# Performance work log

Hardware: AMD Instinct MI355X
Metric: run time of the kernel (lower is better)

The kernel has to match this reference:

```python
import jax, jax.numpy as jnp
import numpy as np

WS = 8          # window size -> N = 64
SHIFT = 4       # shift size for shifted windows
FEAT = 32       # feature map H = W at stage 3
C = 512         # channels (SwinV2-B stage 3)
HEADS = 16
B_IMG = 128     # images -> 128 * (32/8)^2 = 2048 windows


def _rel_coords_table():
    # log-spaced continuous relative coords table, SwinV2 style: [(2W-1)^2, 2]
    r = np.arange(-(WS - 1), WS, dtype=np.float32)
    t = np.stack(np.meshgrid(r, r, indexing='ij'), axis=-1)  # [15,15,2]
    t = t / (WS - 1) * 8.0
    t = np.sign(t) * np.log2(np.abs(t) + 1.0) / np.log2(8.0)
    return t.reshape(-1, 2)


def _rel_pos_index():
    c = np.stack(np.meshgrid(np.arange(WS), np.arange(WS), indexing='ij'))  # [2,8,8]
    cf = c.reshape(2, -1)
    rel = (cf[:, :, None] - cf[:, None, :]).transpose(1, 2, 0)  # [64,64,2]
    rel[:, :, 0] += WS - 1
    rel[:, :, 1] += WS - 1
    rel[:, :, 0] *= 2 * WS - 1
    return rel.sum(-1).astype(np.int32)  # [64,64]


def _shift_mask():
    # standard SwinV2 shifted-window attention mask: [nW, N, N] in {0, -100}
    img = np.zeros((FEAT, FEAT), dtype=np.float32)
    cnt = 0
    for hs in (slice(0, -WS), slice(-WS, -SHIFT), slice(-SHIFT, None)):
        for ws in (slice(0, -WS), slice(-WS, -SHIFT), slice(-SHIFT, None)):
            img[hs, ws] = cnt
            cnt += 1
    win = img.reshape(FEAT // WS, WS, FEAT // WS, WS).transpose(0, 2, 1, 3)
    win = win.reshape(-1, WS * WS)  # [nW, 64]
    diff = win[:, None, :] - win[:, :, None]
    return np.where(diff != 0, -100.0, 0.0).astype(np.float32)


def setup_inputs() -> dict:
    key = jax.random.key(0)
    ks = jax.random.split(key, 10)
    nW = (FEAT // WS) ** 2  # 16 windows per image
    Bw = B_IMG * nW         # 2048
    N = WS * WS
    s = 0.02
    return {
        'x': jax.random.normal(ks[0], (Bw, N, C), jnp.float32),
        'mask': jnp.asarray(_shift_mask()),
        'qkv_w': jax.random.normal(ks[1], (3 * C, C), jnp.float32) * s,
        'q_bias': jnp.zeros((C,), jnp.float32),
        'v_bias': jnp.zeros((C,), jnp.float32),
        'logit_scale': jnp.full((HEADS, 1, 1), np.log(10.0), jnp.float32),
        'cpb_w1': jax.random.normal(ks[2], (512, 2), jnp.float32) * s,
        'cpb_b1': jnp.zeros((512,), jnp.float32),
        'cpb_w2': jax.random.normal(ks[3], (HEADS, 512), jnp.float32) * s,
        'proj_w': jax.random.normal(ks[4], (C, C), jnp.float32) * s,
        'proj_b': jnp.zeros((C,), jnp.float32),
        'rel_coords_table': jnp.asarray(_rel_coords_table()),
        'rel_pos_index': jnp.asarray(_rel_pos_index()),
    }


def reference(x, mask, qkv_w, q_bias, v_bias, logit_scale, cpb_w1, cpb_b1,
              cpb_w2, proj_w, proj_b, rel_coords_table, rel_pos_index):
    Bw, N, Cdim = x.shape
    H = logit_scale.shape[0]
    d = Cdim // H
    # qkv projection; k has no bias (SwinV2)
    qkv_bias = jnp.concatenate([q_bias, jnp.zeros_like(q_bias), v_bias])
    qkv = (x @ qkv_w.T + qkv_bias).reshape(Bw, N, 3, H, d).transpose(2, 0, 3, 1, 4)
    q, k, v = qkv[0], qkv[1], qkv[2]  # each [Bw,H,N,d]
    # cosine attention with learned per-head temperature
    qn = q / jnp.maximum(jnp.linalg.norm(q, axis=-1, keepdims=True), 1e-12)
    kn = k / jnp.maximum(jnp.linalg.norm(k, axis=-1, keepdims=True), 1e-12)
    attn = jnp.einsum('bhnd,bhmd->bhnm', qn, kn)
    scale = jnp.exp(jnp.minimum(logit_scale, jnp.log(100.0)))  # [H,1,1]
    attn = attn * scale[None]
    # continuous relative position bias via small MLP over log-spaced coords
    tbl = jax.nn.relu(rel_coords_table @ cpb_w1.T + cpb_b1) @ cpb_w2.T  # [(2W-1)^2,H]
    bias = tbl[rel_pos_index.reshape(-1)].reshape(N, N, H).transpose(2, 0, 1)
    attn = attn + 16.0 * jax.nn.sigmoid(bias)[None]
    # shifted-window mask applied per window group
    nW = mask.shape[0]
    attn = attn.reshape(Bw // nW, nW, H, N, N) + mask[None, :, None]
    attn = jax.nn.softmax(attn.reshape(Bw, H, N, N), axis=-1)
    out = jnp.einsum('bhnm,bhmd->bhnd', attn, v)
    out = out.transpose(0, 2, 1, 3).reshape(Bw, N, Cdim)
    return out @ proj_w.T + proj_b
```

## Files before the change

kernel.cpp:

```cpp
#include <hip/hip_runtime.h>
#include <stdint.h>
#include <stddef.h>


typedef __attribute__((ext_vector_type(8))) short bf16x8;
typedef __attribute__((ext_vector_type(4))) float f32x4;
typedef __attribute__((ext_vector_type(4))) unsigned short us4;
typedef __attribute__((ext_vector_type(8))) unsigned short us8;
typedef unsigned short u16;
typedef unsigned int u32;

#define FENCE() asm volatile("" ::: "memory")
#define WAITV4() asm volatile("s_waitcnt vmcnt(4)" ::: "memory")
#define WAITV3() asm volatile("s_waitcnt vmcnt(3)" ::: "memory")
#define WAITV0() asm volatile("s_waitcnt vmcnt(0)" ::: "memory")
#define WAITL0() asm volatile("s_waitcnt lgkmcnt(0)" ::: "memory")

__device__ __forceinline__ u16 f2bf(float f) {
  union { __bf16 b; u16 u; } cv;
  cv.b = (__bf16)f;
  return cv.u;
}
__device__ __forceinline__ float bf2f(u16 s) {
  return __uint_as_float(((u32)s) << 16);
}
__device__ __forceinline__ void gl_lds16(const void* g, void* l) {
  __builtin_amdgcn_global_load_lds(
      (const __attribute__((address_space(1))) u32*)g,
      (__attribute__((address_space(3))) u32*)l, 16, 0, 0);
}
__device__ __forceinline__ f32x4 mfma16(bf16x8 a, bf16x8 b, f32x4 c) {
  return __builtin_amdgcn_mfma_f32_16x16x32_bf16(a, b, c, 0, 0, 0);
}
__device__ __forceinline__ bf16x8 ldswz(const u16* p, int ks) {
  return *(const bf16x8*)((const u16*)((uintptr_t)p ^ (uintptr_t)(ks << 6)));
}


__global__ void conv_w_kernel(const float* __restrict__ QW, const float* __restrict__ PW,
                              u16* __restrict__ WQB, u16* __restrict__ WPB) {
  int idx = blockIdx.x * 256 + threadIdx.x;
  const int NQ = 1536 * 512 / 4;
  float4 v; u16* dst;
  if (idx < NQ) { v = ((const float4*)QW)[idx]; dst = WQB + (size_t)idx * 4; }
  else { int k = idx - NQ; v = ((const float4*)PW)[k]; dst = WPB + (size_t)k * 4; }
  us4 u; u.x = f2bf(v.x); u.y = f2bf(v.y); u.z = f2bf(v.z); u.w = f2bf(v.w);
  *(us4*)dst = u;
}

__global__ void xconv_kernel(const float* __restrict__ X, u16* __restrict__ XB) {
  size_t idx = (size_t)blockIdx.x * 256 + threadIdx.x;
  float4 a = ((const float4*)X)[idx * 2];
  float4 b = ((const float4*)X)[idx * 2 + 1];
  us8 o;
  o[0] = f2bf(a.x); o[1] = f2bf(a.y); o[2] = f2bf(a.z); o[3] = f2bf(a.w);
  o[4] = f2bf(b.x); o[5] = f2bf(b.y); o[6] = f2bf(b.z); o[7] = f2bf(b.w);
  *(us8*)&XB[idx * 8] = o;
}

__global__ void sig16_kernel(const float* __restrict__ CT, const float* __restrict__ W1,
                             const float* __restrict__ B1, const float* __restrict__ W2,
                             float* __restrict__ SIG) {
  int i = blockIdx.x;
  int tid = threadIdx.x;
  float c0 = CT[i * 2 + 0], c1 = CT[i * 2 + 1];
  float a[16];
  #pragma unroll
  for (int hh = 0; hh < 16; ++hh) a[hh] = 0.f;
  #pragma unroll
  for (int jj = 0; jj < 2; ++jj) {
    int j = tid + jj * 256;
    float h = fmaxf(c0 * W1[j * 2 + 0] + c1 * W1[j * 2 + 1] + B1[j], 0.f);
    #pragma unroll
    for (int hh = 0; hh < 16; ++hh) a[hh] += h * W2[hh * 512 + j];
  }
  __shared__ float red[4][16];
  #pragma unroll
  for (int hh = 0; hh < 16; ++hh) {
    float v = a[hh];
    for (int m = 1; m < 64; m <<= 1) v += __shfl_xor(v, m);
    if ((tid & 63) == 0) red[tid >> 6][hh] = v;
  }
  __syncthreads();
  if (tid < 16) {
    float v = red[0][tid] + red[1][tid] + red[2][tid] + red[3][tid];
    SIG[i * 16 + tid] = 16.f / (1.f + __expf(-v));
  }
}

__global__ void cmb_kernel(const float* __restrict__ SIG, const float* __restrict__ MASK,
                           const int* __restrict__ RPI, float* __restrict__ CMB) {
  int b = blockIdx.x;
  int w = b >> 4, h = b & 15;
  int tid = threadIdx.x;
  const float* mrow = &MASK[(size_t)w * 4096];
  float* crow = &CMB[(size_t)b * 4096];
  #pragma unroll
  for (int it = 0; it < 16; ++it) {
    int nm = it * 256 + tid;
    crow[nm] = SIG[RPI[nm] * 16 + h] + mrow[nm];
  }
}


#define GEMM32_KLOOP()                                                     \
  _Pragma("unroll")                                                        \
  for (int t = 0; t < 16; ++t) {                                           \
    const int Sb = (t % 3) * 12288;                                        \
    _Pragma("unroll")                                                      \
    for (int m = 0; m < 4; ++m)                                            \
      af[m] = *(const bf16x8*)&S[Sb + (wm * 64 + m * 16 + fr) * 32 + fsw]; \
    _Pragma("unroll")                                                      \
    for (int n = 0; n < 2; ++n)                                            \
      bf[n] = *(const bf16x8*)&S[Sb + 4096 + (wn * 64 + n * 16 + fr) * 32 + fsw]; \
    if (t + 2 <= 15) stageB(t + 2);                                        \
    FENCE(); __builtin_amdgcn_s_barrier(); FENCE();                        \
    WAITL0(); __builtin_amdgcn_sched_barrier(0);                           \
    __builtin_amdgcn_s_setprio(1);                                         \
    _Pragma("unroll")                                                      \
    for (int m = 0; m < 4; ++m)                                            \
      _Pragma("unroll")                                                    \
      for (int n = 0; n < 2; ++n)                                          \
        acc[m][n] = mfma16(af[m], bf[n], acc[m][n]);                       \
    __builtin_amdgcn_s_setprio(0);                                         \
    FENCE(); __builtin_amdgcn_s_barrier(); FENCE();                        \
    _Pragma("unroll")                                                      \
    for (int n = 0; n < 2; ++n)                                            \
      bf[n] = *(const bf16x8*)&S[Sb + 4096 + (wn * 64 + (n + 2) * 16 + fr) * 32 + fsw]; \
    if (t + 3 <= 15) stageA(t + 3);                                        \
    if (t <= 12) { WAITV4(); }                                             \
    else if (t == 13) { WAITV3(); }                                        \
    else if (t == 14) { WAITV0(); }                                        \
    FENCE(); __builtin_amdgcn_s_barrier(); FENCE();                        \
    WAITL0(); __builtin_amdgcn_sched_barrier(0);                           \
    __builtin_amdgcn_s_setprio(1);                                         \
    _Pragma("unroll")                                                      \
    for (int m = 0; m < 4; ++m)                                            \
      _Pragma("unroll")                                                    \
      for (int n = 0; n < 2; ++n)                                          \
        acc[m][n + 2] = mfma16(af[m], bf[n], acc[m][n + 2]);               \
    __builtin_amdgcn_s_setprio(0);                                         \
    FENCE(); __builtin_amdgcn_s_barrier(); FENCE();                        \
  }


__global__ __launch_bounds__(512, 4) void qkv_g32(
    const u16* __restrict__ XB, const u16* __restrict__ WB,
    const float* __restrict__ QB, const float* __restrict__ VB,
    u16* __restrict__ QKV) {
  __shared__ u16 S[36864];
  const int tid = threadIdx.x, lane = tid & 63, w = tid >> 6;
  int bid = blockIdx.x;
  int swz = (bid & 7) * 768 + (bid >> 3);
  const int mt = swz / 6, nt = swz - mt * 6;
  const long m0 = (long)mt * 128, n0 = (long)nt * 256;
  const int wm = w >> 2, wn = w & 3;
  const int fr = lane & 15, lg = lane >> 4;
  const int fsw = (lg ^ ((fr >> 1) & 3)) << 3;
  const f32x4 zf = {0.f, 0.f, 0.f, 0.f};

  f32x4 acc[4][4];
  #pragma unroll
  for (int mi = 0; mi < 4; ++mi)
    #pragma unroll
    for (int ni = 0; ni < 4; ++ni) acc[mi][ni] = zf;

  const int arow = tid >> 2;
  const int asc = (tid & 3) ^ ((arow >> 1) & 3);
  const u16* aSrc = &XB[(size_t)(m0 + arow) * 512 + asc * 8];
  const u16* bSrc0 = &WB[(size_t)(n0 + arow) * 512 + asc * 8];
  const u16* bSrc1 = &WB[(size_t)(n0 + 128 + arow) * 512 + asc * 8];

  auto stageA = [&](int kt) {
    gl_lds16(aSrc + kt * 32, &S[(kt % 3) * 12288 + w * 512]);
  };
  auto stageB = [&](int kt) {
    gl_lds16(bSrc0 + kt * 32, &S[(kt % 3) * 12288 + 4096 + w * 512]);
    gl_lds16(bSrc1 + kt * 32, &S[(kt % 3) * 12288 + 8192 + w * 512]);
  };

  bf16x8 af[4], bf[2];

  stageA(0); stageB(0); stageA(1); stageB(1); stageA(2);
  WAITV4();
  FENCE(); __builtin_amdgcn_s_barrier(); FENCE();

  GEMM32_KLOOP()

  u16* eb = &S[w * 4608];
  #pragma unroll
  for (int ni = 0; ni < 4; ++ni) {
    const long c = n0 + wn * 64 + ni * 16 + fr;
    float bias = (c < 512) ? QB[c] : (c < 1024 ? 0.f : VB[c - 1024]);
    #pragma unroll
    for (int mi = 0; mi < 4; ++mi)
      #pragma unroll
      for (int r = 0; r < 4; ++r)
        eb[(mi * 16 + lg * 4 + r) * 72 + ni * 16 + fr] = f2bf(acc[mi][ni][r] + bias);
  }
  WAITL0();
  #pragma unroll
  for (int i = 0; i < 8; ++i) {
    int row = i * 8 + (lane >> 3);
    int c16 = lane & 7;
    us8 v = *(const us8*)&eb[row * 72 + c16 * 8];
    *(us8*)&QKV[(size_t)(m0 + wm * 64 + row) * 1536 + n0 + wn * 64 + c16 * 8] = v;
  }
}


__global__ __launch_bounds__(512, 4) void proj_g32(
    const u16* __restrict__ A, const u16* __restrict__ WB,
    const float* __restrict__ PB, float* __restrict__ OUT) {
  __shared__ u16 S[36864];
  const int tid = threadIdx.x, lane = tid & 63, w = tid >> 6;
  int bid = blockIdx.x;
  int swz = (bid & 7) * 256 + (bid >> 3);
  const int mt = swz >> 1, nt = swz & 1;
  const long m0 = (long)mt * 128, n0 = (long)nt * 256;
  const int wm = w >> 2, wn = w & 3;
  const int fr = lane & 15, lg = lane >> 4;
  const int fsw = (lg ^ ((fr >> 1) & 3)) << 3;
  const f32x4 zf = {0.f, 0.f, 0.f, 0.f};

  f32x4 acc[4][4];
  #pragma unroll
  for (int mi = 0; mi < 4; ++mi)
    #pragma unroll
    for (int ni = 0; ni < 4; ++ni) acc[mi][ni] = zf;

  const int arow = tid >> 2;
  const int asc = (tid & 3) ^ ((arow >> 1) & 3);
  const u16* aSrc = &A[(size_t)(m0 + arow) * 1536 + asc * 8];
  const u16* bSrc0 = &WB[(size_t)(n0 + arow) * 512 + asc * 8];
  const u16* bSrc1 = &WB[(size_t)(n0 + 128 + arow) * 512 + asc * 8];

  auto stageA = [&](int kt) {
    gl_lds16(aSrc + kt * 32, &S[(kt % 3) * 12288 + w * 512]);
  };
  auto stageB = [&](int kt) {
    gl_lds16(bSrc0 + kt * 32, &S[(kt % 3) * 12288 + 4096 + w * 512]);
    gl_lds16(bSrc1 + kt * 32, &S[(kt % 3) * 12288 + 8192 + w * 512]);
  };

  bf16x8 af[4], bf[2];

  stageA(0); stageB(0); stageA(1); stageB(1); stageA(2);
  WAITV4();
  FENCE(); __builtin_amdgcn_s_barrier(); FENCE();

  GEMM32_KLOOP()

  #pragma unroll
  for (int ni = 0; ni < 4; ++ni) {
    const long c = n0 + wn * 64 + ni * 16 + fr;
    float bias = PB[c];
    #pragma unroll
    for (int mi = 0; mi < 4; ++mi)
      #pragma unroll
      for (int r = 0; r < 4; ++r) {
        long row = m0 + wm * 64 + mi * 16 + lg * 4 + r;
        OUT[row * 512 + c] = acc[mi][ni][r] + bias;
      }
  }
}


__global__ __launch_bounds__(256, 2) void qkv_gemm_rs(
    const float* __restrict__ X, const u16* __restrict__ WB,
    const float* __restrict__ QB, const float* __restrict__ VB,
    u16* __restrict__ QKV) {
  __shared__ u16 As[128 * 64];
  __shared__ u16 Bs[128 * 64];
  const int tid = threadIdx.x, lane = tid & 63, w = tid >> 6;
  int bid = blockIdx.x;
  int swz = (bid & 7) * 1536 + (bid >> 3);
  const int mt = swz / 12, nt = swz - mt * 12;
  const long m0 = (long)mt * 128, n0 = (long)nt * 128;
  const int wm = w >> 1, wn = w & 1;
  const f32x4 zf = {0.f, 0.f, 0.f, 0.f};

  f32x4 acc[4][4];
  #pragma unroll
  for (int mi = 0; mi < 4; ++mi)
    #pragma unroll
    for (int ni = 0; ni < 4; ++ni) acc[mi][ni] = zf;

  const int fr = lane & 15;
  const int fsw = ((lane >> 4) ^ (lane & 7)) * 8;
  const u16* Ap = &As[(wm * 64 + fr) * 64 + fsw];
  const u16* Bp = &Bs[(wn * 64 + fr) * 64 + fsw];

  for (int t = 0; t < 8; ++t) {
    float4 av[8];
    #pragma unroll
    for (int i = 0; i < 8; ++i) {
      int ch = tid + (i << 8);
      int row = ch >> 4, kc = ch & 15;
      av[i] = *(const float4*)&X[(m0 + row) * 512 + t * 64 + kc * 4];
    }
    #pragma unroll
    for (int i = 0; i < 4; ++i) {
      int ch = ((w << 2) + i) * 64 + lane;
      int row = ch >> 3, kc = (ch & 7) ^ (row & 7);
      gl_lds16(&WB[(n0 + row) * 512 + t * 64 + kc * 8], &Bs[((w << 2) + i) * 512]);
    }
    #pragma unroll
    for (int i = 0; i < 8; ++i) {
      int ch = tid + (i << 8);
      int row = ch >> 4, kc = ch & 15;
      int kcs = kc ^ ((row & 7) << 1);
      us4 u; u.x = f2bf(av[i].x); u.y = f2bf(av[i].y); u.z = f2bf(av[i].z); u.w = f2bf(av[i].w);
      *(us4*)&As[row * 64 + kcs * 4] = u;
    }
    __syncthreads();
    #pragma unroll
    for (int ks = 0; ks < 2; ++ks) {
      bf16x8 af[4], bfr[4];
      #pragma unroll
      for (int mi = 0; mi < 4; ++mi) af[mi] = ldswz(Ap + mi * 1024, ks);
      #pragma unroll
      for (int ni = 0; ni < 4; ++ni) bfr[ni] = ldswz(Bp + ni * 1024, ks);
      #pragma unroll
      for (int mi = 0; mi < 4; ++mi)
        #pragma unroll
        for (int ni = 0; ni < 4; ++ni)
          acc[mi][ni] = mfma16(af[mi], bfr[ni], acc[mi][ni]);
    }
    __syncthreads();
  }

  #pragma unroll
  for (int ni = 0; ni < 4; ++ni) {
    const long c = n0 + wn * 64 + ni * 16 + (lane & 15);
    float bias = (c < 512) ? QB[c] : (c < 1024 ? 0.f : VB[c - 1024]);
    #pragma unroll
    for (int mi = 0; mi < 4; ++mi)
      #pragma unroll
      for (int r = 0; r < 4; ++r) {
        long row = m0 + wm * 64 + mi * 16 + (lane >> 4) * 4 + r;
        QKV[row * 1536 + c] = f2bf(acc[mi][ni][r] + bias);
      }
  }
}


__global__ __launch_bounds__(256, 4) void attn_kernel(
    u16* __restrict__ QKV, const float* __restrict__ CMB, const float* __restrict__ LS) {
  __shared__ u16 sm[7424];
  u16* qs = sm;
  u16* ksm = sm + 2560;
  u16* ps = sm;
  u16* vt = sm + 5120;
  const int tid = threadIdx.x, lane = tid & 63, w = tid >> 6;
  const int b = blockIdx.x, wi = b & 15;
  const size_t base = (size_t)b * 64 * 1536;
  const int cl = lane & 15, lg = lane >> 4;
  const int srow = tid >> 2, sck = tid & 3;
  const int vd = tid & 31, vkb = tid >> 5;
  const f32x4 zf = {0.f, 0.f, 0.f, 0.f};

  for (int h = 0; h < 16; ++h) {
    const float scale = __expf(fminf(LS[h], 4.6051702f));
    {
      us8 qv = *(const us8*)&QKV[base + (size_t)srow * 1536 + h * 32 + sck * 8];
      float qf[8]; float ss = 0.f;
      #pragma unroll
      for (int j = 0; j < 8; ++j) { qf[j] = bf2f(qv[j]); ss += qf[j] * qf[j]; }
      ss += __shfl_xor(ss, 1); ss += __shfl_xor(ss, 2);
      float rn = scale / fmaxf(sqrtf(ss), 1e-12f);
      us8 qo;
      #pragma unroll
      for (int j = 0; j < 8; ++j) qo[j] = f2bf(qf[j] * rn);
      *(us8*)&qs[srow * 40 + sck * 8] = qo;
    }
    {
      us8 kv = *(const us8*)&QKV[base + (size_t)srow * 1536 + 512 + h * 32 + sck * 8];
      float kf[8]; float ss = 0.f;
      #pragma unroll
      for (int j = 0; j < 8; ++j) { kf[j] = bf2f(kv[j]); ss += kf[j] * kf[j]; }
      ss += __shfl_xor(ss, 1); ss += __shfl_xor(ss, 2);
      float rn = 1.f / fmaxf(sqrtf(ss), 1e-12f);
      us8 ko;
      #pragma unroll
      for (int j = 0; j < 8; ++j) ko[j] = f2bf(kf[j] * rn);
      *(us8*)&ksm[srow * 40 + sck * 8] = ko;
    }
    {
      us8 vo;
      #pragma unroll
      for (int e = 0; e < 8; ++e)
        vo[e] = QKV[base + (size_t)(vkb * 8 + e) * 1536 + 1024 + h * 32 + vd];
      *(us8*)&vt[vd * 72 + vkb * 8] = vo;
    }
    __syncthreads();

    bf16x8 aq = *(const bf16x8*)&qs[(w * 16 + cl) * 40 + lg * 8];
    f32x4 s4[4];
    #pragma unroll
    for (int nt = 0; nt < 4; ++nt) {
      bf16x8 bk = *(const bf16x8*)&ksm[(nt * 16 + cl) * 40 + lg * 8];
      s4[nt] = mfma16(aq, bk, zf);
    }

    const float* cp = &CMB[((size_t)(wi * 16 + h)) << 12];
    const int r0 = w * 16 + lg * 4;
    float p[4][4];
    #pragma unroll
    for (int r = 0; r < 4; ++r) {
      float mx = -3.0e38f;
      #pragma unroll
      for (int q4 = 0; q4 < 4; ++q4) {
        float v = s4[q4][r] + cp[(r0 + r) * 64 + q4 * 16 + cl];
        p[q4][r] = v; mx = fmaxf(mx, v);
      }
      mx = fmaxf(mx, __shfl_xor(mx, 1));
      mx = fmaxf(mx, __shfl_xor(mx, 2));
      mx = fmaxf(mx, __shfl_xor(mx, 4));
      mx = fmaxf(mx, __shfl_xor(mx, 8));
      float sum = 0.f;
      #pragma unroll
      for (int q4 = 0; q4 < 4; ++q4) { float e = __expf(p[q4][r] - mx); p[q4][r] = e; sum += e; }
      sum += __shfl_xor(sum, 1); sum += __shfl_xor(sum, 2);
      sum += __shfl_xor(sum, 4); sum += __shfl_xor(sum, 8);
      float inv = 1.f / sum;
      #pragma unroll
      for (int q4 = 0; q4 < 4; ++q4) p[q4][r] *= inv;
    }
    __syncthreads();

    #pragma unroll
    for (int r = 0; r < 4; ++r)
      #pragma unroll
      for (int q4 = 0; q4 < 4; ++q4)
        ps[(r0 + r) * 72 + q4 * 16 + cl] = f2bf(p[q4][r]);

    f32x4 o4[2]; o4[0] = zf; o4[1] = zf;
    #pragma unroll
    for (int ks = 0; ks < 2; ++ks) {
      bf16x8 ap = *(const bf16x8*)&ps[(w * 16 + cl) * 72 + ks * 32 + lg * 8];
      #pragma unroll
      for (int n2 = 0; n2 < 2; ++n2) {
        bf16x8 bv = *(const bf16x8*)&vt[(n2 * 16 + cl) * 72 + ks * 32 + lg * 8];
        o4[n2] = mfma16(ap, bv, o4[n2]);
      }
    }
    #pragma unroll
    for (int n2 = 0; n2 < 2; ++n2)
      #pragma unroll
      for (int r = 0; r < 4; ++r)
        QKV[base + (size_t)(w * 16 + lg * 4 + r) * 1536 + h * 32 + n2 * 16 + cl] = f2bf(o4[n2][r]);
    __syncthreads();
  }
}


extern "C" void kernel_launch(void* const* d_in, const int* in_sizes, int n_in,
                              void* d_out, int out_size, void* d_ws, size_t ws_size,
                              hipStream_t stream) {
  const float* X    = (const float*)d_in[0];
  const float* MASK = (const float*)d_in[1];
  const float* QW   = (const float*)d_in[2];
  const float* QB   = (const float*)d_in[3];
  const float* VB   = (const float*)d_in[4];
  const float* LS   = (const float*)d_in[5];
  const float* CW1  = (const float*)d_in[6];
  const float* CB1  = (const float*)d_in[7];
  const float* CW2  = (const float*)d_in[8];
  const float* PW   = (const float*)d_in[9];
  const float* PB   = (const float*)d_in[10];
  const float* CT   = (const float*)d_in[11];
  const int*   RPI  = (const int*)d_in[12];
  float* OUT = (float*)d_out;

  char* ws = (char*)d_ws;
  const bool big = ws_size >= 543178752ull;
  u16* QKV = (u16*)ws;
  u16* XB  = (u16*)(ws + 402653184ull);
  size_t off = big ? 536870912ull : 402653184ull;
  float* CMB = (float*)(ws + off);  off += 4194304ull;
  float* SIG = (float*)(ws + off);  off += 16384ull;
  u16*   WQB = (u16*)(ws + off);    off += 1572864ull;
  u16*   WPB = (u16*)(ws + off);

  conv_w_kernel<<<1024, 256, 0, stream>>>(QW, PW, WQB, WPB);
  sig16_kernel<<<225, 256, 0, stream>>>(CT, CW1, CB1, CW2, SIG);
  cmb_kernel<<<256, 256, 0, stream>>>(SIG, MASK, RPI, CMB);
  if (big) {
    xconv_kernel<<<32768, 256, 0, stream>>>(X, XB);
    qkv_g32<<<6144, 512, 0, stream>>>(XB, WQB, QB, VB, QKV);
  } else {
    qkv_gemm_rs<<<12288, 256, 0, stream>>>(X, WQB, QB, VB, QKV);
  }
  attn_kernel<<<2048, 256, 0, stream>>>(QKV, CMB, LS);
  proj_g32<<<2048, 512, 0, stream>>>(QKV, WPB, PB, OUT);
}
```

Measured before the change: 641.9 us.

## Assign one head per wavefront in attention, removing block-wide syncs

The attention kernel is restructured so each wavefront owns a whole (window, head) pair: 4 heads per block, 8192 blocks, instead of one block looping over 16 heads with 4 waves splitting rows. Q/K are loaded and normalized directly into MFMA register fragments, the bias/mask is preloaded into the accumulators, and only P and V^T go through per-wave LDS, so all __syncthreads are dropped. This aims to remove the serial head loop and barrier stalls, and to expose more parallelism and overlap of memory latency. In exchange, register pressure and LDS use go up (launch bounds lowered to 3 blocks per CU), and V is transposed through scalar LDS writes.

```diff
diff --git a/kernel.cpp b/kernel.cpp
--- a/kernel.cpp
+++ b/kernel.cpp
@@ -345,113 +345,124 @@
 }
 
 
-__global__ __launch_bounds__(256, 4) void attn_kernel(
+__global__ __launch_bounds__(256, 3) void attn_wh(
     u16* __restrict__ QKV, const float* __restrict__ CMB, const float* __restrict__ LS) {
-  __shared__ u16 sm[7424];
-  u16* qs = sm;
-  u16* ksm = sm + 2560;
-  u16* ps = sm;
-  u16* vt = sm + 5120;
+  __shared__ u16 smu[26112];
   const int tid = threadIdx.x, lane = tid & 63, w = tid >> 6;
-  const int b = blockIdx.x, wi = b & 15;
-  const size_t base = (size_t)b * 64 * 1536;
-  const int cl = lane & 15, lg = lane >> 4;
-  const int srow = tid >> 2, sck = tid & 3;
-  const int vd = tid & 31, vkb = tid >> 5;
+  const int b = blockIdx.x;
+  const int win = b >> 2;
+  const int h = (b & 3) * 4 + w;
+  const int wi = win & 15;
+  const size_t base = (size_t)win * 64 * 1536;
+  const int fr = lane & 15, lg = lane >> 4;
+  u16* ps = &smu[w * 6528];
+  u16* vt = ps + 4352;
+  const float scale = __expf(fminf(LS[h], 4.6051702f));
+  const float* cp = &CMB[((size_t)(wi * 16 + h)) << 12];
   const f32x4 zf = {0.f, 0.f, 0.f, 0.f};
 
-  for (int h = 0; h < 16; ++h) {
-    const float scale = __expf(fminf(LS[h], 4.6051702f));
-    {
-      us8 qv = *(const us8*)&QKV[base + (size_t)srow * 1536 + h * 32 + sck * 8];
-      float qf[8]; float ss = 0.f;
-      #pragma unroll
-      for (int j = 0; j < 8; ++j) { qf[j] = bf2f(qv[j]); ss += qf[j] * qf[j]; }
-      ss += __shfl_xor(ss, 1); ss += __shfl_xor(ss, 2);
-      float rn = scale / fmaxf(sqrtf(ss), 1e-12f);
-      us8 qo;
-      #pragma unroll
-      for (int j = 0; j < 8; ++j) qo[j] = f2bf(qf[j] * rn);
-      *(us8*)&qs[srow * 40 + sck * 8] = qo;
-    }
-    {
-      us8 kv = *(const us8*)&QKV[base + (size_t)srow * 1536 + 512 + h * 32 + sck * 8];
-      float kf[8]; float ss = 0.f;
-      #pragma unroll
-      for (int j = 0; j < 8; ++j) { kf[j] = bf2f(kv[j]); ss += kf[j] * kf[j]; }
-      ss += __shfl_xor(ss, 1); ss += __shfl_xor(ss, 2);
-      float rn = 1.f / fmaxf(sqrtf(ss), 1e-12f);
-      us8 ko;
-      #pragma unroll
-      for (int j = 0; j < 8; ++j) ko[j] = f2bf(kf[j] * rn);
-      *(us8*)&ksm[srow * 40 + sck * 8] = ko;
-    }
-    {
-      us8 vo;
-      #pragma unroll
-      for (int e = 0; e < 8; ++e)
-        vo[e] = QKV[base + (size_t)(vkb * 8 + e) * 1536 + 1024 + h * 32 + vd];
-      *(us8*)&vt[vd * 72 + vkb * 8] = vo;
-    }
-    __syncthreads();
-
-    bf16x8 aq = *(const bf16x8*)&qs[(w * 16 + cl) * 40 + lg * 8];
-    f32x4 s4[4];
-    #pragma unroll
-    for (int nt = 0; nt < 4; ++nt) {
-      bf16x8 bk = *(const bf16x8*)&ksm[(nt * 16 + cl) * 40 + lg * 8];
-      s4[nt] = mfma16(aq, bk, zf);
-    }
-
-    const float* cp = &CMB[((size_t)(wi * 16 + h)) << 12];
-    const int r0 = w * 16 + lg * 4;
-    float p[4][4];
+  us8 vrow[4];
+  #pragma unroll
+  for (int c = 0; c < 4; ++c)
+    vrow[c] = *(const us8*)&QKV[base + (size_t)lane * 1536 + 1024 + h * 32 + c * 8];
+
+  f32x4 acc[4][4];
+  #pragma unroll
+  for (int m = 0; m < 4; ++m)
+    #pragma unroll
+    for (int n = 0; n < 4; ++n)
+      #pragma unroll
+      for (int r = 0; r < 4; ++r)
+        acc[m][n][r] = cp[(m * 16 + lg * 4 + r) * 64 + n * 16 + fr];
+
+  bf16x8 af[4], bk[4];
+  #pragma unroll
+  for (int m = 0; m < 4; ++m) {
+    us8 qv = *(const us8*)&QKV[base + (size_t)(m * 16 + fr) * 1536 + h * 32 + lg * 8];
+    float qf[8]; float ss = 0.f;
+    #pragma unroll
+    for (int j = 0; j < 8; ++j) { qf[j] = bf2f(qv[j]); ss += qf[j] * qf[j]; }
+    ss += __shfl_xor(ss, 16); ss += __shfl_xor(ss, 32);
+    float rn = scale / fmaxf(sqrtf(ss), 1e-12f);
+    union { us8 u; bf16x8 b; } cv;
+    #pragma unroll
+    for (int j = 0; j < 8; ++j) cv.u[j] = f2bf(qf[j] * rn);
+    af[m] = cv.b;
+  }
+  #pragma unroll
+  for (int m = 0; m < 4; ++m) {
+    us8 kv = *(const us8*)&QKV[base + (size_t)(m * 16 + fr) * 1536 + 512 + h * 32 + lg * 8];
+    float kf[8]; float ss = 0.f;
+    #pragma unroll
+    for (int j = 0; j < 8; ++j) { kf[j] = bf2f(kv[j]); ss += kf[j] * kf[j]; }
+    ss += __shfl_xor(ss, 16); ss += __shfl_xor(ss, 32);
+    float rn = 1.f / fmaxf(sqrtf(ss), 1e-12f);
+    union { us8 u; bf16x8 b; } cv;
+    #pragma unroll
+    for (int j = 0; j < 8; ++j) cv.u[j] = f2bf(kf[j] * rn);
+    bk[m] = cv.b;
+  }
+
+  #pragma unroll
+  for (int m = 0; m < 4; ++m)
+    #pragma unroll
+    for (int n = 0; n < 4; ++n)
+      acc[m][n] = mfma16(af[m], bk[n], acc[m][n]);
+
+  #pragma unroll
+  for (int c = 0; c < 4; ++c)
+    #pragma unroll
+    for (int j = 0; j < 8; ++j)
+      vt[(c * 8 + j) * 68 + lane] = vrow[c][j];
+
+  #pragma unroll
+  for (int m = 0; m < 4; ++m)
     #pragma unroll
     for (int r = 0; r < 4; ++r) {
+      float pv[4];
       float mx = -3.0e38f;
       #pragma unroll
-      for (int q4 = 0; q4 < 4; ++q4) {
-        float v = s4[q4][r] + cp[(r0 + r) * 64 + q4 * 16 + cl];
-        p[q4][r] = v; mx = fmaxf(mx, v);
-      }
+      for (int n = 0; n < 4; ++n) { pv[n] = acc[m][n][r]; mx = fmaxf(mx, pv[n]); }
       mx = fmaxf(mx, __shfl_xor(mx, 1));
       mx = fmaxf(mx, __shfl_xor(mx, 2));
       mx = fmaxf(mx, __shfl_xor(mx, 4));
       mx = fmaxf(mx, __shfl_xor(mx, 8));
       float sum = 0.f;
       #pragma unroll
-      for (int q4 = 0; q4 < 4; ++q4) { float e = __expf(p[q4][r] - mx); p[q4][r] = e; sum += e; }
+      for (int n = 0; n < 4; ++n) { pv[n] = __expf(pv[n] - mx); sum += pv[n]; }
       sum += __shfl_xor(sum, 1); sum += __shfl_xor(sum, 2);
       sum += __shfl_xor(sum, 4); sum += __shfl_xor(sum, 8);
       float inv = 1.f / sum;
       #pragma unroll
-      for (int q4 = 0; q4 < 4; ++q4) p[q4][r] *= inv;
+      for (int n = 0; n < 4; ++n)
+        ps[(m * 16 + lg * 4 + r) * 68 + n * 16 + fr] = f2bf(pv[n] * inv);
     }
-    __syncthreads();
-
-    #pragma unroll
-    for (int r = 0; r < 4; ++r)
-      #pragma unroll
-      for (int q4 = 0; q4 < 4; ++q4)
-        ps[(r0 + r) * 72 + q4 * 16 + cl] = f2bf(p[q4][r]);
-
-    f32x4 o4[2]; o4[0] = zf; o4[1] = zf;
+
+  WAITL0(); __builtin_amdgcn_sched_barrier(0);
+
+  f32x4 o[4][2];
+  #pragma unroll
+  for (int m = 0; m < 4; ++m) { o[m][0] = zf; o[m][1] = zf; }
+  #pragma unroll
+  for (int m = 0; m < 4; ++m)
     #pragma unroll
     for (int ks = 0; ks < 2; ++ks) {
-      bf16x8 ap = *(const bf16x8*)&ps[(w * 16 + cl) * 72 + ks * 32 + lg * 8];
+      bf16x8 ap = *(const bf16x8*)&ps[(m * 16 + fr) * 68 + ks * 32 + lg * 8];
       #pragma unroll
       for (int n2 = 0; n2 < 2; ++n2) {
-        bf16x8 bv = *(const bf16x8*)&vt[(n2 * 16 + cl) * 72 + ks * 32 + lg * 8];
-        o4[n2] = mfma16(ap, bv, o4[n2]);
+        bf16x8 bv = *(const bf16x8*)&vt[(n2 * 16 + fr) * 68 + ks * 32 + lg * 8];
+        o[m][n2] = mfma16(ap, bv, o[m][n2]);
       }
     }
+
+  #pragma unroll
+  for (int m = 0; m < 4; ++m)
     #pragma unroll
     for (int n2 = 0; n2 < 2; ++n2)
       #pragma unroll
       for (int r = 0; r < 4; ++r)
-        QKV[base + (size_t)(w * 16 + lg * 4 + r) * 1536 + h * 32 + n2 * 16 + cl] = f2bf(o4[n2][r]);
-    __syncthreads();
-  }
+        QKV[base + (size_t)(m * 16 + lg * 4 + r) * 1536 + h * 32 + n2 * 16 + fr] =
+            f2bf(o[m][n2][r]);
 }
 
 
@@ -492,6 +503,6 @@
   } else {
     qkv_gemm_rs<<<12288, 256, 0, stream>>>(X, WQB, QB, VB, QKV);
   }
-  attn_kernel<<<2048, 256, 0, stream>>>(QKV, CMB, LS);
+  attn_wh<<<8192, 256, 0, stream>>>(QKV, CMB, LS);
   proj_g32<<<2048, 512, 0, stream>>>(QKV, WPB, PB, OUT);
 }
```

Measured after the change: 641.7 us. About the same (-0.0%).
